# Optimization experiments

Measured on AMD Instinct MI355X. Metric: run time of the kernel, lower is better.

The kernel has to match this reference:

```python
import jax, jax.numpy as jnp
import numpy as np

N, D = 66560, 128      # total actor rows, embedding dim
M = 16384              # anchor count (scenes x vehicles)
P, NEG = 3, 63         # positives per anchor, negatives per anchor
EPS = 1e-8             # torch nn.CosineSimilarity eps


def setup_inputs() -> dict:
    key = jax.random.key(0)
    k1, k2, k3, k4, k5 = jax.random.split(key, 5)
    return {
        "ids_fut": jax.random.normal(k1, (N, D), dtype=jnp.float32),
        "ids_hist": jax.random.normal(k2, (N, D), dtype=jnp.float32),
        "anchor_idx": jax.random.randint(k3, (M,), 0, N),
        "pos_idx": jax.random.randint(k4, (M, P), 0, N),
        "neg_idx": jax.random.randint(k5, (M, NEG), 0, N),
    }


def _cos_plus_one(anchor, samples):
    # anchor: [M, D], samples: [M, K, D] -> cosine sim + 1, per torch CosineSimilarity
    dot = jnp.einsum("md,mkd->mk", anchor, samples)
    na = jnp.linalg.norm(anchor, axis=-1)[:, None]          # [M, 1]
    ns = jnp.linalg.norm(samples, axis=-1)                  # [M, K]
    return dot / jnp.maximum(na * ns, EPS) + 1.0


def reference(ids_fut, ids_hist, anchor_idx, pos_idx, neg_idx):
    anchor = ids_hist[anchor_idx]          # [M, D]
    pos = ids_fut[pos_idx]                 # [M, P, D]
    neg = ids_fut[neg_idx]                 # [M, NEG, D]
    sp = jnp.sum(_cos_plus_one(anchor, pos), axis=1)   # [M]
    sn = jnp.sum(_cos_plus_one(anchor, neg), axis=1)   # [M]
    sim_loss = -jnp.log(sp / (sp + sn))                 # [M]
    loss_tot = jnp.sum(sim_loss)           # 'repres_loss'; 'repres_loss_cnt' == M (constant)
    return loss_tot
```

## Files before the change

kernel.cpp:

```cpp
#include <hip/hip_runtime.h>
#include <math.h>

#define DIM 128
#define P_POS 3
#define N_NEG 63
#define SCALE 16.0f

typedef float floatx2 __attribute__((ext_vector_type(2)));

#if defined(__has_builtin)
#if __has_builtin(__builtin_elementwise_fma)
#define HAVE_EFMA 1
#endif
#endif

__device__ __forceinline__ floatx2 pkfma(floatx2 a, floatx2 b, floatx2 c) {
#ifdef HAVE_EFMA
    return __builtin_elementwise_fma(a, b, c);
#else
    floatx2 r;
    r.x = fmaf(a.x, b.x, c.x);
    r.y = fmaf(a.y, b.y, c.y);
    return r;
#endif
}

__device__ __forceinline__ float wave_reduce_sum(float v) {
#pragma unroll
    for (int off = 32; off > 0; off >>= 1) v += __shfl_xor(v, off, 64);
    return v;
}
__device__ __forceinline__ float g16_reduce(float v) {
#pragma unroll
    for (int off = 8; off > 0; off >>= 1) v += __shfl_xor(v, off, 64);
    return v;
}
__device__ __forceinline__ float g32_reduce(float v) {
#pragma unroll
    for (int off = 16; off > 0; off >>= 1) v += __shfl_xor(v, off, 64);
    return v;
}

__global__ __launch_bounds__(256) void prep_fp8_kernel(const float* __restrict__ fut,
                                                       unsigned* __restrict__ futq,
                                                       int nrows) {
    int half = threadIdx.x >> 5;
    int l = threadIdx.x & 31;
    int row = blockIdx.x * 8 + half;
    if (row >= nrows) return;
    float4 x = *reinterpret_cast<const float4*>(fut + (size_t)row * DIM + l * 4);
    float ss = x.x * x.x;
    ss = fmaf(x.y, x.y, ss);
    ss = fmaf(x.z, x.z, ss);
    ss = fmaf(x.w, x.w, ss);
    ss = g32_reduce(ss);
    float r = (ss > 0.f) ? rsqrtf(ss) * SCALE : 0.f;
    int w = __builtin_amdgcn_cvt_pk_fp8_f32(x.x * r, x.y * r, 0, false);
    w = __builtin_amdgcn_cvt_pk_fp8_f32(x.z * r, x.w * r, w, true);
    futq[(size_t)row * 32 + l] = (unsigned)w;
}

__global__ __launch_bounds__(256) void idloss_fp8p_kernel(
    const float* __restrict__ hist, const int* __restrict__ anchor_idx,
    const int* __restrict__ pos_idx, const int* __restrict__ neg_idx,
    const uint2* __restrict__ futq, float* __restrict__ partials) {
    __shared__ float smem[4];
    const int wave = threadIdx.x >> 6;
    const int lane = threadIdx.x & 63;
    const int m = __builtin_amdgcn_readfirstlane(blockIdx.x * 4 + wave);
    const int g = lane >> 4;
    const int t = lane & 15;

    int nidx = (lane < N_NEG) ? neg_idx[m * N_NEG + lane] : 0;

    const int aidx = anchor_idx[m];
    const int p0 = pos_idx[m * P_POS + 0];
    const int p1 = pos_idx[m * P_POS + 1];
    const int p2 = pos_idx[m * P_POS + 2];
    int pidx = (g == 1) ? p1 : (g == 2) ? p2 : p0;

    const float4* ap =
        reinterpret_cast<const float4*>(hist + (size_t)aidx * DIM + t * 8);
    float4 a0 = ap[0], a1 = ap[1];
    float ss = a0.x * a0.x;
    ss = fmaf(a0.y, a0.y, ss);
    ss = fmaf(a0.z, a0.z, ss);
    ss = fmaf(a0.w, a0.w, ss);
    ss = fmaf(a1.x, a1.x, ss);
    ss = fmaf(a1.y, a1.y, ss);
    ss = fmaf(a1.z, a1.z, ss);
    ss = fmaf(a1.w, a1.w, ss);
    ss = g16_reduce(ss);
    float rna = (ss > 0.f) ? rsqrtf(ss) * (1.0f / SCALE) : 0.f;
    floatx2 av0, av1, av2, av3;
    av0.x = a0.x * rna; av0.y = a0.y * rna;
    av1.x = a0.z * rna; av1.y = a0.w * rna;
    av2.x = a1.x * rna; av2.y = a1.y * rna;
    av3.x = a1.z * rna; av3.y = a1.w * rna;

    int js[16];
#pragma unroll
    for (int k = 0; k < 16; ++k) js[k] = __shfl(nidx, 4 * k + g, 64);

    uint2 vp = futq[(size_t)pidx * 16 + t];
    if (g >= P_POS) { vp.x = 0u; vp.y = 0u; }
    uint2 vs[16];
#pragma unroll
    for (int k = 0; k < 16; ++k) {
        vs[k] = futq[(size_t)js[k] * 16 + t];
        if (4 * k + g >= N_NEG) { vs[k].x = 0u; vs[k].y = 0u; }
    }

    floatx2 na = {0.f, 0.f}, nb = {0.f, 0.f};
#pragma unroll
    for (int k = 0; k < 16; ++k) {
        uint2 v = vs[k];
        na = pkfma(__builtin_amdgcn_cvt_pk_f32_fp8(v.x, false), av0, na);
        nb = pkfma(__builtin_amdgcn_cvt_pk_f32_fp8(v.x, true), av1, nb);
        na = pkfma(__builtin_amdgcn_cvt_pk_f32_fp8(v.y, false), av2, na);
        nb = pkfma(__builtin_amdgcn_cvt_pk_f32_fp8(v.y, true), av3, nb);
    }
    floatx2 pa = {0.f, 0.f};
    pa = pkfma(__builtin_amdgcn_cvt_pk_f32_fp8(vp.x, false), av0, pa);
    pa = pkfma(__builtin_amdgcn_cvt_pk_f32_fp8(vp.x, true), av1, pa);
    pa = pkfma(__builtin_amdgcn_cvt_pk_f32_fp8(vp.y, false), av2, pa);
    pa = pkfma(__builtin_amdgcn_cvt_pk_f32_fp8(vp.y, true), av3, pa);

    float accn = wave_reduce_sum(na.x + na.y + nb.x + nb.y);
    float accp = wave_reduce_sum(pa.x + pa.y);

    if (lane == 0) {
        float sp = accp + (float)P_POS;
        float sn = accn + (float)N_NEG;
        smem[wave] = -logf(sp / (sp + sn));
    }
    __syncthreads();
    if (threadIdx.x == 0)
        partials[blockIdx.x] = smem[0] + smem[1] + smem[2] + smem[3];
}

__global__ __launch_bounds__(256) void reduce_kernel(const float* __restrict__ partials,
                                                     float* __restrict__ out, int n) {
    __shared__ float smem[256];
    float acc = 0.f;
    for (int i = threadIdx.x; i < n; i += 256) acc += partials[i];
    smem[threadIdx.x] = acc;
    __syncthreads();
#pragma unroll
    for (int s = 128; s > 0; s >>= 1) {
        if ((int)threadIdx.x < s) smem[threadIdx.x] += smem[threadIdx.x + s];
        __syncthreads();
    }
    if (threadIdx.x == 0) out[0] = smem[0];
}

extern "C" void kernel_launch(void* const* d_in, const int* in_sizes, int n_in,
                              void* d_out, int out_size, void* d_ws, size_t ws_size,
                              hipStream_t stream) {
    const float* fut  = (const float*)d_in[0];
    const float* hist = (const float*)d_in[1];
    const int* anchor_idx = (const int*)d_in[2];
    const int* pos_idx    = (const int*)d_in[3];
    const int* neg_idx    = (const int*)d_in[4];

    int N = in_sizes[0] / DIM;
    int M = in_sizes[2];
    int main_blocks = M / 4;

    size_t futq_bytes = (size_t)N * 32 * sizeof(unsigned);
    unsigned* futq = (unsigned*)d_ws;
    float* partials = (float*)((char*)d_ws + futq_bytes);

    int prep_blocks = (N + 7) / 8;
    prep_fp8_kernel<<<prep_blocks, 256, 0, stream>>>(fut, futq, N);
    idloss_fp8p_kernel<<<main_blocks, 256, 0, stream>>>(hist, anchor_idx, pos_idx,
                                                        neg_idx, (const uint2*)futq,
                                                        partials);
    reduce_kernel<<<1, 256, 0, stream>>>(partials, (float*)d_out, main_blocks);
}
```

Baseline: 34.12 us.

## Map each sample row across the whole wave with 2-byte fp8 loads

Changes the work split inside a wave. Before, 4 lane groups of 16 each read 8 bytes per row, with indices shuffled between lanes. Now all 64 lanes each read 2 bytes of one row at a time, with sample indices loaded as wave-uniform scalars, and four rows are accumulated in flight. It also drops the block-level shared-memory combine: each wave writes its own partial, so the final reduction covers M entries. Narrower per-lane loads may raise instruction count and reduce memory-level parallelism, in exchange for removing the shuffles and masking.

```diff
diff --git a/kernel.cpp b/kernel.cpp
--- a/kernel.cpp
+++ b/kernel.cpp
@@ -30,11 +30,6 @@
     for (int off = 32; off > 0; off >>= 1) v += __shfl_xor(v, off, 64);
     return v;
 }
-__device__ __forceinline__ float g16_reduce(float v) {
-#pragma unroll
-    for (int off = 8; off > 0; off >>= 1) v += __shfl_xor(v, off, 64);
-    return v;
-}
 __device__ __forceinline__ float g32_reduce(float v) {
 #pragma unroll
     for (int off = 16; off > 0; off >>= 1) v += __shfl_xor(v, off, 64);
@@ -60,83 +55,67 @@
     futq[(size_t)row * 32 + l] = (unsigned)w;
 }
 
-__global__ __launch_bounds__(256) void idloss_fp8p_kernel(
+__global__ __launch_bounds__(256) void idloss_sb_kernel(
     const float* __restrict__ hist, const int* __restrict__ anchor_idx,
     const int* __restrict__ pos_idx, const int* __restrict__ neg_idx,
-    const uint2* __restrict__ futq, float* __restrict__ partials) {
-    __shared__ float smem[4];
+    const unsigned short* __restrict__ futq, float* __restrict__ partials) {
     const int wave = threadIdx.x >> 6;
     const int lane = threadIdx.x & 63;
     const int m = __builtin_amdgcn_readfirstlane(blockIdx.x * 4 + wave);
-    const int g = lane >> 4;
-    const int t = lane & 15;
 
-    int nidx = (lane < N_NEG) ? neg_idx[m * N_NEG + lane] : 0;
+    const int* __restrict__ nb = neg_idx + m * N_NEG;
+    const int* __restrict__ pb = pos_idx + m * P_POS;
 
     const int aidx = anchor_idx[m];
-    const int p0 = pos_idx[m * P_POS + 0];
-    const int p1 = pos_idx[m * P_POS + 1];
-    const int p2 = pos_idx[m * P_POS + 2];
-    int pidx = (g == 1) ? p1 : (g == 2) ? p2 : p0;
+    float2 a = *reinterpret_cast<const float2*>(hist + (size_t)aidx * DIM + lane * 2);
+    float ss = wave_reduce_sum(fmaf(a.x, a.x, a.y * a.y));
+    float rna = (ss > 0.f) ? rsqrtf(ss) * (1.0f / SCALE) : 0.f;
+    floatx2 av;
+    av.x = a.x * rna;
+    av.y = a.y * rna;
 
-    const float4* ap =
-        reinterpret_cast<const float4*>(hist + (size_t)aidx * DIM + t * 8);
-    float4 a0 = ap[0], a1 = ap[1];
-    float ss = a0.x * a0.x;
-    ss = fmaf(a0.y, a0.y, ss);
-    ss = fmaf(a0.z, a0.z, ss);
-    ss = fmaf(a0.w, a0.w, ss);
-    ss = fmaf(a1.x, a1.x, ss);
-    ss = fmaf(a1.y, a1.y, ss);
-    ss = fmaf(a1.z, a1.z, ss);
-    ss = fmaf(a1.w, a1.w, ss);
-    ss = g16_reduce(ss);
-    float rna = (ss > 0.f) ? rsqrtf(ss) * (1.0f / SCALE) : 0.f;
-    floatx2 av0, av1, av2, av3;
-    av0.x = a0.x * rna; av0.y = a0.y * rna;
-    av1.x = a0.z * rna; av1.y = a0.w * rna;
-    av2.x = a1.x * rna; av2.y = a1.y * rna;
-    av3.x = a1.z * rna; av3.y = a1.w * rna;
-
-    int js[16];
+    floatx2 accp = {0.f, 0.f};
 #pragma unroll
-    for (int k = 0; k < 16; ++k) js[k] = __shfl(nidx, 4 * k + g, 64);
-
-    uint2 vp = futq[(size_t)pidx * 16 + t];
-    if (g >= P_POS) { vp.x = 0u; vp.y = 0u; }
-    uint2 vs[16];
-#pragma unroll
-    for (int k = 0; k < 16; ++k) {
-        vs[k] = futq[(size_t)js[k] * 16 + t];
-        if (4 * k + g >= N_NEG) { vs[k].x = 0u; vs[k].y = 0u; }
+    for (int j = 0; j < P_POS; ++j) {
+        int s = pb[j];
+        int v = (int)futq[(size_t)s * 64 + lane];
+        accp = pkfma(__builtin_amdgcn_cvt_pk_f32_fp8(v, false), av, accp);
     }
 
-    floatx2 na = {0.f, 0.f}, nb = {0.f, 0.f};
+    floatx2 n0 = {0.f, 0.f}, n1 = {0.f, 0.f}, n2 = {0.f, 0.f}, n3 = {0.f, 0.f};
 #pragma unroll
-    for (int k = 0; k < 16; ++k) {
-        uint2 v = vs[k];
-        na = pkfma(__builtin_amdgcn_cvt_pk_f32_fp8(v.x, false), av0, na);
-        nb = pkfma(__builtin_amdgcn_cvt_pk_f32_fp8(v.x, true), av1, nb);
-        na = pkfma(__builtin_amdgcn_cvt_pk_f32_fp8(v.y, false), av2, na);
-        nb = pkfma(__builtin_amdgcn_cvt_pk_f32_fp8(v.y, true), av3, nb);
+    for (int j = 0; j < 60; j += 4) {
+        int s0 = nb[j + 0], s1 = nb[j + 1], s2 = nb[j + 2], s3 = nb[j + 3];
+        int v0 = (int)futq[(size_t)s0 * 64 + lane];
+        int v1 = (int)futq[(size_t)s1 * 64 + lane];
+        int v2 = (int)futq[(size_t)s2 * 64 + lane];
+        int v3 = (int)futq[(size_t)s3 * 64 + lane];
+        n0 = pkfma(__builtin_amdgcn_cvt_pk_f32_fp8(v0, false), av, n0);
+        n1 = pkfma(__builtin_amdgcn_cvt_pk_f32_fp8(v1, false), av, n1);
+        n2 = pkfma(__builtin_amdgcn_cvt_pk_f32_fp8(v2, false), av, n2);
+        n3 = pkfma(__builtin_amdgcn_cvt_pk_f32_fp8(v3, false), av, n3);
     }
-    floatx2 pa = {0.f, 0.f};
-    pa = pkfma(__builtin_amdgcn_cvt_pk_f32_fp8(vp.x, false), av0, pa);
-    pa = pkfma(__builtin_amdgcn_cvt_pk_f32_fp8(vp.x, true), av1, pa);
-    pa = pkfma(__builtin_amdgcn_cvt_pk_f32_fp8(vp.y, false), av2, pa);
-    pa = pkfma(__builtin_amdgcn_cvt_pk_f32_fp8(vp.y, true), av3, pa);
+    {
+        int s0 = nb[60], s1 = nb[61], s2 = nb[62];
+        int v0 = (int)futq[(size_t)s0 * 64 + lane];
+        int v1 = (int)futq[(size_t)s1 * 64 + lane];
+        int v2 = (int)futq[(size_t)s2 * 64 + lane];
+        n0 = pkfma(__builtin_amdgcn_cvt_pk_f32_fp8(v0, false), av, n0);
+        n1 = pkfma(__builtin_amdgcn_cvt_pk_f32_fp8(v1, false), av, n1);
+        n2 = pkfma(__builtin_amdgcn_cvt_pk_f32_fp8(v2, false), av, n2);
+    }
 
-    float accn = wave_reduce_sum(na.x + na.y + nb.x + nb.y);
-    float accp = wave_reduce_sum(pa.x + pa.y);
+    floatx2 ns = n0 + n1;
+    floatx2 ns2 = n2 + n3;
+    ns = ns + ns2;
+    float accn = wave_reduce_sum(ns.x + ns.y);
+    float accpf = wave_reduce_sum(accp.x + accp.y);
 
     if (lane == 0) {
-        float sp = accp + (float)P_POS;
+        float sp = accpf + (float)P_POS;
         float sn = accn + (float)N_NEG;
-        smem[wave] = -logf(sp / (sp + sn));
+        partials[m] = -logf(sp / (sp + sn));
     }
-    __syncthreads();
-    if (threadIdx.x == 0)
-        partials[blockIdx.x] = smem[0] + smem[1] + smem[2] + smem[3];
 }
 
 __global__ __launch_bounds__(256) void reduce_kernel(const float* __restrict__ partials,
@@ -173,8 +152,9 @@
 
     int prep_blocks = (N + 7) / 8;
     prep_fp8_kernel<<<prep_blocks, 256, 0, stream>>>(fut, futq, N);
-    idloss_fp8p_kernel<<<main_blocks, 256, 0, stream>>>(hist, anchor_idx, pos_idx,
-                                                        neg_idx, (const uint2*)futq,
-                                                        partials);
-    reduce_kernel<<<1, 256, 0, stream>>>(partials, (float*)d_out, main_blocks);
+    idloss_sb_kernel<<<main_blocks, 256, 0, stream>>>(hist, anchor_idx, pos_idx,
+                                                      neg_idx,
+                                                      (const unsigned short*)futq,
+                                                      partials);
+    reduce_kernel<<<1, 256, 0, stream>>>(partials, (float*)d_out, M);
 }
```

Result: slower. 46.54 us (+36.4%).
